# Performance work log

Hardware: AMD Instinct MI355X
Metric: run time of the kernel (lower is better)

The kernel has to match this reference:

```python
import jax, jax.numpy as jnp
import numpy as np

# Model constants (from source: model_dim=1024, head_dim=128, num_heads=8)
L = 8          # num layers (reduced from 16 for tractable reference memory)
T = 2048       # packed tokens, B == 1 (varlen)
DIM = 1024
NH = 8
NKV = 4        # GQA kv heads
HD = 128
KVD = NKV * HD
BLOCK = 128
WS = 3
WIN = WS * BLOCK           # sliding-window size for 'S' layers
ATTN_SCALE = 0.12
PATTERN = 'SSSL'
GATE_CH = 32
EPS = 1.1920929e-07        # torch F.rms_norm default eps = finfo(fp32).eps


def rms_norm(x):
    return x * jax.lax.rsqrt(jnp.mean(x * x, axis=-1, keepdims=True) + EPS)


def apply_rotary(x, cos, sin):
    # x: [T, H, HD]; cos/sin: [T, 1, HD//2]
    d = x.shape[-1] // 2
    x1, x2 = x[..., :d], x[..., d:]
    return jnp.concatenate([x1 * cos + x2 * sin, -x1 * sin + x2 * cos], axis=-1)


def has_ve(layer_idx, n_layer):
    return layer_idx % 2 == (n_layer - 1) % 2


def setup_inputs() -> dict:
    key = jax.random.key(0)
    ks = jax.random.split(key, 9)
    x = jax.random.normal(ks[0], (1, T, DIM), jnp.float32)
    ve = jax.random.normal(ks[1], (L, T, KVD), jnp.float32)
    s = DIM ** -0.5
    Wq = jax.random.normal(ks[2], (L, DIM, NH * HD), jnp.float32) * s
    Wk = jax.random.normal(ks[3], (L, DIM, KVD), jnp.float32) * s
    Wv = jax.random.normal(ks[4], (L, DIM, KVD), jnp.float32) * s
    Wo = jax.random.normal(ks[5], (L, NH * HD, DIM), jnp.float32) * (NH * HD) ** -0.5
    Wgate = jax.random.normal(ks[6], (L, GATE_CH, NKV), jnp.float32) * GATE_CH ** -0.5
    Wfc = jax.random.normal(ks[7], (L, DIM, 4 * DIM), jnp.float32) * s
    Wproj = jax.random.normal(ks[8], (L, 4 * DIM, DIM), jnp.float32) * (4 * DIM) ** -0.5
    # RoPE tables (absolute positions of the packed batch, as in the source)
    inv_freq = 1.0 / (10000.0 ** (jnp.arange(HD // 2, dtype=jnp.float32) / (HD // 2)))
    ang = jnp.arange(T, dtype=jnp.float32)[:, None] * inv_freq[None, :]
    cos = jnp.cos(ang)[:, None, :]
    sin = jnp.sin(ang)[:, None, :]
    # cu_seqlens: 4 packed documents of 512 tokens
    seqlens = jnp.array([0, 512, 1024, 1536, 2048], dtype=jnp.int32)
    return dict(x=x, ve=ve, Wq=Wq, Wk=Wk, Wv=Wv, Wo=Wo, Wgate=Wgate,
                Wfc=Wfc, Wproj=Wproj, cos=cos, sin=sin, seqlens=seqlens)


def reference(x, ve, Wq, Wk, Wv, Wo, Wgate, Wfc, Wproj, cos, sin, seqlens):
    h = x[0]  # [T, DIM], B == 1 (varlen packing)
    pos = jnp.arange(T)
    doc = jnp.searchsorted(seqlens, pos, side='right') - 1
    diff = pos[:, None] - pos[None, :]
    base = (diff >= 0) & (doc[:, None] == doc[None, :])   # causal within doc
    mask_S = base & (diff <= WIN)                         # sliding window
    neg = jnp.float32(-1e30)
    rep = NH // NKV
    for l in range(L):
        xn = rms_norm(h)
        q = (xn @ Wq[l]).reshape(T, NH, HD)
        k = (xn @ Wk[l]).reshape(T, NKV, HD)
        v = (xn @ Wv[l]).reshape(T, NKV, HD)
        if has_ve(l, L):
            gate = 2.0 * jax.nn.sigmoid(xn[:, :GATE_CH] @ Wgate[l])  # [T, NKV]
            v = v + gate[:, :, None] * ve[l].reshape(T, NKV, HD)
        q = rms_norm(apply_rotary(q, cos, sin))
        k = rms_norm(apply_rotary(k, cos, sin))
        k = jnp.repeat(k, rep, axis=1)   # GQA -> full heads
        v2 = jnp.repeat(v, rep, axis=1)
        scores = jnp.einsum('thd,shd->hts', q, k) * ATTN_SCALE  # [NH, T, T]
        mask = mask_S if PATTERN[l % len(PATTERN)] == 'S' else base
        scores = jnp.where(mask[None], scores, neg)
        p = jax.nn.softmax(scores, axis=-1)
        y = jnp.einsum('hts,shd->thd', p, v2).reshape(T, NH * HD)
        h = h + y @ Wo[l]
        m = jnp.square(jax.nn.relu(rms_norm(h) @ Wfc[l]))  # relu(x)^2 MLP
        h = h + m @ Wproj[l]
    return h[None]
```

## Files before the change

### kernel.cpp

```cpp
#include <hip/hip_runtime.h>
#include <hip/hip_bf16.h>
#include <cstdint>
#include <cstddef>

#define TT     2048
#define DMODEL 1024
#define NHQ    8
#define HD     128
#define KVD    512
#define WIN    384
#define EPSF   1.1920929e-07f
#define SCALE  0.12f

typedef __attribute__((ext_vector_type(8))) short bf16x8;
typedef __attribute__((ext_vector_type(4))) float f32x4;

#define WAITV(N)  asm volatile("s_waitcnt vmcnt(" #N ")" ::: "memory")

__device__ __forceinline__ float b2f(unsigned short u) {
    unsigned int i = ((unsigned int)u) << 16; float f; __builtin_memcpy(&f, &i, 4); return f;
}
__device__ __forceinline__ unsigned short f2b(float f) {
    unsigned int i; __builtin_memcpy(&i, &f, 4);
    unsigned int r = (i + 0x7fffu + ((i >> 16) & 1u)) >> 16;
    return (unsigned short)r;
}

__device__ __forceinline__ void gl_lds16(const unsigned short* g, unsigned short* l) {
    __builtin_amdgcn_global_load_lds(
        (const __attribute__((address_space(1))) unsigned int*)g,
        (__attribute__((address_space(3))) unsigned int*)l, 16, 0, 0);
}
__device__ __forceinline__ void gl_lds16f(const float* g, float* l) {
    __builtin_amdgcn_global_load_lds(
        (const __attribute__((address_space(1))) unsigned int*)g,
        (__attribute__((address_space(3))) unsigned int*)l, 16, 0, 0);
}

__global__ __launch_bounds__(512)
void convT_k(const float* __restrict__ Wq, const float* __restrict__ Wk,
             const float* __restrict__ Wv, const float* __restrict__ Wo,
             const float* __restrict__ Wfc, const float* __restrict__ Wproj,
             unsigned short* __restrict__ Bqkv, unsigned short* __restrict__ Bo,
             unsigned short* __restrict__ Bfc, unsigned short* __restrict__ Bproj)
{
    __shared__ float lt[128 * 128];
    const int bid = blockIdx.x, tid = threadIdx.x, l = blockIdx.y;

    const float* W; unsigned short* Wt; int K, N, t, nbase;
    if (bid < 64)         { W = Wq    + (size_t)l * 1024 * 1024; Wt = Bqkv  + (size_t)l * 2048 * 1024; K = 1024; N = 1024; t = bid;       nbase = 0;    }
    else if (bid < 96)    { W = Wk    + (size_t)l * 1024 * 512;  Wt = Bqkv  + (size_t)l * 2048 * 1024; K = 1024; N = 512;  t = bid - 64;  nbase = 1024; }
    else if (bid < 128)   { W = Wv    + (size_t)l * 1024 * 512;  Wt = Bqkv  + (size_t)l * 2048 * 1024; K = 1024; N = 512;  t = bid - 96;  nbase = 1536; }
    else if (bid < 192)   { W = Wo    + (size_t)l * 1024 * 1024; Wt = Bo    + (size_t)l * 1024 * 1024; K = 1024; N = 1024; t = bid - 128; nbase = 0;    }
    else if (bid < 448)   { W = Wfc   + (size_t)l * 1024 * 4096; Wt = Bfc   + (size_t)l * 4096 * 1024; K = 1024; N = 4096; t = bid - 192; nbase = 0;    }
    else                  { W = Wproj + (size_t)l * 4096 * 1024; Wt = Bproj + (size_t)l * 1024 * 4096; K = 4096; N = 1024; t = bid - 448; nbase = 0;    }

    const int ktiles = K >> 7;
    const int kt0 = (t % ktiles) * 128, nt0 = (t / ktiles) * 128;

    const int lane = tid & 63, w = tid >> 6;
    const int lhi = lane >> 5;
    const int lc  = lane & 31;

    #pragma unroll
    for (int rd = 0; rd < 8; ++rd) {
        const int k = rd * 16 + w * 2 + lhi;
        const int csrc = lc ^ ((k >> 3) & 31);
        const float* src = W + (size_t)(kt0 + k) * N + nt0 + csrc * 4;
        float* dst = lt + (size_t)(rd * 16 + w * 2) * 128;
        gl_lds16f(src, dst);
    }
    __syncthreads();

    #pragma unroll
    for (int i = 0; i < 4; ++i) {
        int flat = i * 512 + tid;
        int n = flat >> 4, kc = (flat & 15) * 8;
        const int c = ((n >> 2) ^ (kc >> 3)) & 31;
        const float* rp = lt + (size_t)kc * 128 + c * 4 + (n & 3);
        unsigned short o[8];
        #pragma unroll
        for (int j = 0; j < 8; ++j) o[j] = f2b(rp[j * 128]);
        *(uint4*)(Wt + (size_t)(nbase + nt0 + n) * K + kt0 + kc) = *(const uint4*)o;
    }
}

template<int EPI>
__global__ __launch_bounds__(256, 2)
void gemm4(const unsigned short* __restrict__ A, const unsigned short* __restrict__ Bt,
           unsigned short* __restrict__ Cp, int K, int ksplit, int Ntot)
{
    __shared__ unsigned short As[2 * 128 * 64];
    __shared__ unsigned short Bs[2 * 128 * 64];
    const int BUF = 128 * 64;
    const int tid = threadIdx.x, lane = tid & 63, wv = tid >> 6;

    const int gx = gridDim.x;
    const int nwg = gx * gridDim.y;
    const int ihw = blockIdx.y * gx + blockIdx.x;
    const int q = nwg >> 3, r = nwg & 7;
    const int xcd = ihw & 7, pos = ihw >> 3;
    const int lg = (xcd < r) ? xcd * (q + 1) + pos
                             : r * (q + 1) + (xcd - r) * q + pos;
    const int m0 = (lg % gx) * 128, n0 = (lg / gx) * 128;

    const int kbeg = blockIdx.z * ksplit;
    const int NT = ksplit >> 6;

    const int wr = (wv >> 1) * 64, wc = (wv & 1) * 64;
    const int l15 = lane & 15, g = lane >> 4;
    const int srow = lane >> 3;
    const int sxor = (((lane & 7) ^ srow) << 3);

    const unsigned short* gA0 = A  + (size_t)(m0 + wv * 32 + srow) * K + sxor;
    const unsigned short* gB0 = Bt + (size_t)(n0 + wv * 32 + srow) * K + sxor;

    auto stage = [&](int t) {
        const int b = t & 1;
        const size_t k = (size_t)kbeg + ((size_t)t << 6);
        unsigned short* la = As + b * BUF + (wv * 32) * 64;
        unsigned short* lb = Bs + b * BUF + (wv * 32) * 64;
        #pragma unroll
        for (int c = 0; c < 4; ++c) {
            gl_lds16(gA0 + (size_t)(c * 8) * K + k, la + c * 8 * 64);
            gl_lds16(gB0 + (size_t)(c * 8) * K + k, lb + c * 8 * 64);
        }
    };

    f32x4 acc[4][4] = {};

    stage(0);
    for (int t = 0; t < NT; ++t) {
        if (t + 1 < NT) { stage(t + 1); WAITV(8); }
        else            { WAITV(0); }
        __builtin_amdgcn_s_barrier();

        const unsigned short* Ac = As + (t & 1) * BUF;
        const unsigned short* Bc = Bs + (t & 1) * BUF;
        bf16x8 af[4][2], bfv[4][2];
        #pragma unroll
        for (int mi = 0; mi < 4; ++mi) {
            const int row = wr + mi * 16 + l15, x = row & 7;
            #pragma unroll
            for (int kk = 0; kk < 2; ++kk)
                af[mi][kk] = *(const bf16x8*)(Ac + row * 64 + (((kk * 4 + g) ^ x) << 3));
        }
        #pragma unroll
        for (int ni = 0; ni < 4; ++ni) {
            const int row = wc + ni * 16 + l15, x = row & 7;
            #pragma unroll
            for (int kk = 0; kk < 2; ++kk)
                bfv[ni][kk] = *(const bf16x8*)(Bc + row * 64 + (((kk * 4 + g) ^ x) << 3));
        }
        __builtin_amdgcn_s_setprio(1);
        #pragma unroll
        for (int kk = 0; kk < 2; ++kk)
            #pragma unroll
            for (int mi = 0; mi < 4; ++mi)
                #pragma unroll
                for (int ni = 0; ni < 4; ++ni)
                    acc[mi][ni] = __builtin_amdgcn_mfma_f32_16x16x32_bf16(af[mi][kk], bfv[ni][kk], acc[mi][ni], 0, 0, 0);
        __builtin_amdgcn_s_setprio(0);
        __builtin_amdgcn_s_barrier();
    }

    unsigned short* Cz = Cp + (size_t)blockIdx.z * TT * Ntot;
    #pragma unroll
    for (int mi = 0; mi < 4; ++mi)
        #pragma unroll
        for (int ni = 0; ni < 4; ++ni)
            #pragma unroll
            for (int r2 = 0; r2 < 4; ++r2) {
                int row = m0 + wr + mi * 16 + g * 4 + r2;
                int col = n0 + wc + ni * 16 + l15;
                size_t idx = (size_t)row * Ntot + col;
                float v = acc[mi][ni][r2];
                if (EPI == 0) Cz[idx] = f2b(v);
                else {
                    float z = v > 0.f ? v * v : 0.f;
                    Cz[idx] = f2b(z);
                }
            }
}

__global__ __launch_bounds__(256)
void rmsnormF_k(float* __restrict__ h, const unsigned short* __restrict__ part, int nz,
                unsigned short* __restrict__ xn)
{
    const int t = blockIdx.x, tid = threadIdx.x;
    const size_t idx = (size_t)t * (DMODEL / 4) + tid;
    float4 v = ((const float4*)h)[idx];
    for (int z = 0; z < nz; ++z) {
        ushort4 p = ((const ushort4*)part)[idx + (size_t)z * (TT * DMODEL / 4)];
        v.x += b2f(p.x); v.y += b2f(p.y); v.z += b2f(p.z); v.w += b2f(p.w);
    }
    if (nz > 0) ((float4*)h)[idx] = v;

    float ss = v.x*v.x + v.y*v.y + v.z*v.z + v.w*v.w;
    #pragma unroll
    for (int m = 1; m < 64; m <<= 1) ss += __shfl_xor(ss, m);
    __shared__ float red[4];
    if ((tid & 63) == 0) red[tid >> 6] = ss;
    __syncthreads();
    float tot = red[0] + red[1] + red[2] + red[3];
    float rs = rsqrtf(tot * (1.f / DMODEL) + EPSF);
    unsigned short o[4] = { f2b(v.x*rs), f2b(v.y*rs), f2b(v.z*rs), f2b(v.w*rs) };
    *(ushort4*)(xn + (size_t)t * DMODEL + tid * 4) = *(const ushort4*)o;
}

__global__ __launch_bounds__(256)
void reduce_add_k(float* __restrict__ h, const unsigned short* __restrict__ part, int nz)
{
    const int i = blockIdx.x * 256 + threadIdx.x;
    float4 hv = ((float4*)h)[i];
    for (int z = 0; z < nz; ++z) {
        ushort4 p = ((const ushort4*)part)[i + (size_t)z * (TT * DMODEL / 4)];
        hv.x += b2f(p.x); hv.y += b2f(p.y); hv.z += b2f(p.z); hv.w += b2f(p.w);
    }
    ((float4*)h)[i] = hv;
}

__global__ __launch_bounds__(128)
void post_qkv_k(const unsigned short* __restrict__ qkv,
                const float* __restrict__ cosb, const float* __restrict__ sinb,
                unsigned short* __restrict__ qn, unsigned short* __restrict__ kn)
{
    const size_t S2 = (size_t)TT * 2048;
    const int t = blockIdx.x, tid = threadIdx.x;
    __shared__ float cs[64], sn[64];
    if (tid < 64) { cs[tid] = cosb[t * 64 + tid]; sn[tid] = sinb[t * 64 + tid]; }
    __syncthreads();
    if (tid < 96) {
        const int hid = tid >> 3, sub = tid & 7;
        const unsigned short* src; unsigned short* dst;
        if (hid < 8) { src = qkv + (size_t)t * 2048 + hid * 128;              dst = qn + (size_t)t * 1024 + hid * 128; }
        else         { src = qkv + (size_t)t * 2048 + 1024 + (hid - 8) * 128; dst = kn + (size_t)t * 512 + (hid - 8) * 128; }
        float o1[8], o2[8], ssum = 0.f;
        #pragma unroll
        for (int j = 0; j < 8; ++j) {
            int jj = sub * 8 + j;
            float x1 = b2f(src[jj])      + b2f(src[jj + S2]);
            float x2 = b2f(src[jj + 64]) + b2f(src[jj + 64 + S2]);
            float c = cs[jj], s = sn[jj];
            o1[j] = x1 * c + x2 * s;
            o2[j] = -x1 * s + x2 * c;
            ssum += o1[j]*o1[j] + o2[j]*o2[j];
        }
        ssum += __shfl_xor(ssum, 1); ssum += __shfl_xor(ssum, 2); ssum += __shfl_xor(ssum, 4);
        float rs = rsqrtf(ssum * (1.f / HD) + EPSF);
        #pragma unroll
        for (int j = 0; j < 8; ++j) {
            int jj = sub * 8 + j;
            dst[jj]      = f2b(o1[j] * rs);
            dst[jj + 64] = f2b(o2[j] * rs);
        }
    }
}

__global__ __launch_bounds__(256)
void vtrans2_k(const unsigned short* __restrict__ qkv, const unsigned short* __restrict__ xn,
               const float* __restrict__ Wgate, const float* __restrict__ vel, int hasve,
               unsigned short* __restrict__ vt)
{
    const size_t S2 = (size_t)TT * 2048;
    __shared__ unsigned short lt[64][72];
    __shared__ float gate_s[64];
    const int t0 = blockIdx.x * 64, c0 = blockIdx.y * 64, tid = threadIdx.x;
    const int gi = c0 >> 7;

    if (hasve && tid < 64) {
        const int t = t0 + tid;
        float a = 0.f;
        #pragma unroll
        for (int c = 0; c < 32; ++c) a += b2f(xn[(size_t)t * DMODEL + c]) * Wgate[c * 4 + gi];
        gate_s[tid] = 2.f / (1.f + __expf(-a));
    }
    __syncthreads();

    #pragma unroll
    for (int i = 0; i < 2; ++i) {
        int r = (tid >> 3) + i * 32;
        int c = (tid & 7) * 8;
        const int t = t0 + r, ch = c0 + c;
        size_t off = (size_t)t * 2048 + 1536 + ch;
        bf16x8 pa = *(const bf16x8*)(qkv + off);
        bf16x8 pb = *(const bf16x8*)(qkv + off + S2);
        float g = hasve ? gate_s[r] : 0.f;
        #pragma unroll
        for (int j = 0; j < 8; ++j) {
            float vv = b2f(((unsigned short*)&pa)[j]) + b2f(((unsigned short*)&pb)[j]);
            if (hasve) vv += g * vel[(size_t)t * KVD + ch + j];
            lt[c + j][r] = f2b(vv);
        }
    }
    __syncthreads();
    #pragma unroll
    for (int i = 0; i < 2; ++i) {
        int r = (tid >> 3) + i * 32;
        int c = (tid & 7) * 8;
        *(bf16x8*)(vt + (size_t)(c0 + r) * TT + t0 + c) = *(const bf16x8*)(&lt[r][c]);
    }
}

__global__ __launch_bounds__(256)
void attn_k(const unsigned short* __restrict__ qn, const unsigned short* __restrict__ kn,
            const unsigned short* __restrict__ vt,
            float* __restrict__ pacc, float* __restrict__ pml,
            const int* __restrict__ seqlens, int isS)
{
    const int tid = threadIdx.x, w = tid >> 6, lane = tid & 63;
    const int h = blockIdx.y, hkv = h >> 1, z = blockIdx.z;
    const int qr = (blockIdx.x * 4 + w) * 16;
    const int s1 = seqlens[1], s2 = seqlens[2], s3 = seqlens[3];
    const int l15 = lane & 15, g = lane >> 4;

    const int row = qr + l15;
    const int drow = (row >= s1) + (row >= s2) + (row >= s3);

    int dq = (qr >= s1) + (qr >= s2) + (qr >= s3);
    int dstart = dq == 0 ? 0 : (dq == 1 ? s1 : (dq == 2 ? s2 : s3));
    int smin = dstart;
    if (isS) { int wlo = qr - WIN; if (wlo > smin) smin = wlo; }
    if (smin < 0) smin = 0;
    const int smax = qr + 16;

    const int base0 = smin & ~31;
    const int ntiles = (smax - base0 + 31) >> 5;
    const int tp = (ntiles + 1) >> 1;
    const int tbeg = z ? tp : 0, tend = z ? ntiles : tp;

    const size_t rowi = ((size_t)z * NHQ + h) * TT + row;

    if (tbeg >= tend) {
        if (lane < 16) { pml[rowi * 2] = -1e30f; pml[rowi * 2 + 1] = 0.f; }
        return;
    }

    bf16x8 qf[4];
    #pragma unroll
    for (int kk = 0; kk < 4; ++kk)
        qf[kk] = *(const bf16x8*)(qn + (size_t)(qr + l15) * 1024 + h * HD + kk * 32 + g * 8);

    f32x4 acc[8] = {};
    float mrow = -1e30f, lrow = 0.f;

    for (int tt = tbeg; tt < tend; ++tt) {
        const int s0 = base0 + tt * 32;
        f32x4 S[2] = {};
        __builtin_amdgcn_s_setprio(1);
        #pragma unroll
        for (int nb = 0; nb < 2; ++nb) {
            int srow = s0 + nb * 16 + l15;
            #pragma unroll
            for (int kk = 0; kk < 4; ++kk) {
                bf16x8 kf = *(const bf16x8*)(kn + (size_t)srow * KVD + hkv * HD + kk * 32 + g * 8);
                S[nb] = __builtin_amdgcn_mfma_f32_16x16x32_bf16(kf, qf[kk], S[nb], 0, 0, 0);
            }
        }
        __builtin_amdgcn_s_setprio(0);

        float sv[2][4];
        #pragma unroll
        for (int nb = 0; nb < 2; ++nb)
            #pragma unroll
            for (int r = 0; r < 4; ++r) {
                int s = s0 + nb * 16 + 4 * g + r;
                int dcol = (s >= s1) + (s >= s2) + (s >= s3);
                bool valid = (s <= row) && (dcol == drow) && (!isS || (row - s) <= WIN);
                sv[nb][r] = valid ? S[nb][r] * SCALE : -1e30f;
            }

        float pm = sv[0][0];
        #pragma unroll
        for (int r = 1; r < 4; ++r) pm = fmaxf(pm, sv[0][r]);
        #pragma unroll
        for (int r = 0; r < 4; ++r) pm = fmaxf(pm, sv[1][r]);
        pm = fmaxf(pm, __shfl_xor(pm, 16));
        pm = fmaxf(pm, __shfl_xor(pm, 32));
        float mnew = fmaxf(mrow, pm);
        const float vany = (mnew > -1e29f) ? 1.f : 0.f;
        float scl2 = __expf(mrow - mnew);
        float p0[4], p1[4], ps = 0.f;
        #pragma unroll
        for (int r = 0; r < 4; ++r) {
            p0[r] = vany * __expf(sv[0][r] - mnew);
            p1[r] = vany * __expf(sv[1][r] - mnew);
            ps += p0[r] + p1[r];
        }
        ps += __shfl_xor(ps, 16);
        ps += __shfl_xor(ps, 32);
        lrow = lrow * scl2 + ps;
        mrow = mnew;
        #pragma unroll
        for (int nb2 = 0; nb2 < 8; ++nb2) acc[nb2] *= scl2;

        unsigned short pt[8];
        const int base = l15 + ((g & 1) << 5);
        #pragma unroll
        for (int jh = 0; jh < 2; ++jh)
            #pragma unroll
            for (int r = 0; r < 4; ++r) {
                float ta = __shfl(p0[r], base + 16 * jh);
                float tb = __shfl(p1[r], base + 16 * jh);
                pt[jh * 4 + r] = f2b(g >= 2 ? tb : ta);
            }
        bf16x8 pf;
        #pragma unroll
        for (int j = 0; j < 8; ++j) ((unsigned short*)&pf)[j] = pt[j];

        __builtin_amdgcn_s_setprio(1);
        #pragma unroll
        for (int nb2 = 0; nb2 < 8; ++nb2) {
            bf16x8 vf = *(const bf16x8*)(vt + (size_t)(hkv * HD + nb2 * 16 + l15) * TT + s0 + g * 8);
            acc[nb2] = __builtin_amdgcn_mfma_f32_16x16x32_bf16(vf, pf, acc[nb2], 0, 0, 0);
        }
        __builtin_amdgcn_s_setprio(0);
    }

    float* pa = pacc + rowi * HD;
    #pragma unroll
    for (int nb2 = 0; nb2 < 8; ++nb2)
        *(float4*)(pa + nb2 * 16 + 4 * g) = *(float4*)&acc[nb2];
    if (lane < 16) { pml[rowi * 2] = mrow; pml[rowi * 2 + 1] = lrow; }
}

__global__ __launch_bounds__(256)
void attn_merge_k(const float* __restrict__ pacc, const float* __restrict__ pml,
                  unsigned short* __restrict__ y)
{
    const int r = blockIdx.x, tid = threadIdx.x;
    const int h = tid >> 5, dg = (tid & 31) * 4;
    const size_t i1 = ((size_t)0 * NHQ + h) * TT + r;
    const size_t i2 = ((size_t)1 * NHQ + h) * TT + r;
    const float m1 = pml[i1 * 2], l1 = pml[i1 * 2 + 1];
    const float m2 = pml[i2 * 2], l2 = pml[i2 * 2 + 1];
    const float M = fmaxf(m1, m2);
    const float w1 = (l1 > 0.f) ? __expf(m1 - M) : 0.f;
    const float w2 = (l2 > 0.f) ? __expf(m2 - M) : 0.f;
    const float inv = 1.f / (w1 * l1 + w2 * l2);

    float4 a1 = {0.f, 0.f, 0.f, 0.f}, a2 = {0.f, 0.f, 0.f, 0.f};
    if (l1 > 0.f) a1 = *(const float4*)(pacc + i1 * HD + dg);
    if (l2 > 0.f) a2 = *(const float4*)(pacc + i2 * HD + dg);

    unsigned short o[4];
    o[0] = f2b((w1 * a1.x + w2 * a2.x) * inv);
    o[1] = f2b((w1 * a1.y + w2 * a2.y) * inv);
    o[2] = f2b((w1 * a1.z + w2 * a2.z) * inv);
    o[3] = f2b((w1 * a1.w + w2 * a2.w) * inv);
    *(ushort4*)(y + (size_t)r * 1024 + h * HD + dg) = *(const ushort4*)o;
}

extern "C" void kernel_launch(void* const* d_in, const int* in_sizes, int n_in,
                              void* d_out, int out_size, void* d_ws, size_t ws_size,
                              hipStream_t stream)
{
    const float* x       = (const float*)d_in[0];
    const float* ve      = (const float*)d_in[1];
    const float* Wq      = (const float*)d_in[2];
    const float* Wk      = (const float*)d_in[3];
    const float* Wv      = (const float*)d_in[4];
    const float* Wo      = (const float*)d_in[5];
    const float* Wgate   = (const float*)d_in[6];
    const float* Wfc     = (const float*)d_in[7];
    const float* Wproj   = (const float*)d_in[8];
    const float* cosb    = (const float*)d_in[9];
    const float* sinb    = (const float*)d_in[10];
    const int*   seqlens = (const int*)d_in[11];

    float* h = (float*)d_out;
    char* ws = (char*)d_ws;
    unsigned short* xn    = (unsigned short*)(ws);
    unsigned short* qn    = (unsigned short*)(ws + (4ull  << 20));
    unsigned short* kn    = (unsigned short*)(ws + (8ull  << 20));
    unsigned short* vt    = (unsigned short*)(ws + (12ull << 20));
    unsigned short* yb    = (unsigned short*)(ws + (14ull << 20));
    unsigned short* mb    = (unsigned short*)(ws + (18ull << 20));
    unsigned short* part  = (unsigned short*)(ws + (34ull << 20));
    float*          pacc  = (float*)(ws + (50ull << 20));
    float*          pml   = (float*)(ws + (66ull << 20));
    unsigned short* Bqkv  = (unsigned short*)(ws + (68ull  << 20));
    unsigned short* Bo    = (unsigned short*)(ws + (100ull << 20));
    unsigned short* Bfc   = (unsigned short*)(ws + (116ull << 20));
    unsigned short* Bproj = (unsigned short*)(ws + (180ull << 20));

    hipMemcpyAsync(h, x, (size_t)TT * DMODEL * sizeof(float), hipMemcpyDeviceToDevice, stream);

    convT_k<<<dim3(704, 8), 512, 0, stream>>>(Wq, Wk, Wv, Wo, Wfc, Wproj,
                                              Bqkv, Bo, Bfc, Bproj);

    for (int l = 0; l < 8; ++l) {
        int hasve = (l % 2) == 1;
        int isS   = (l % 4) != 3;

        rmsnormF_k<<<TT, 256, 0, stream>>>(h, part, l == 0 ? 0 : 4, xn);

        gemm4<0><<<dim3(16, 16, 2), 256, 0, stream>>>(xn, Bqkv + (size_t)l * 2048 * 1024,
                                                      part, 1024, 512, 2048);

        post_qkv_k<<<TT, 128, 0, stream>>>(part, cosb, sinb, qn, kn);

        vtrans2_k<<<dim3(32, 8), 256, 0, stream>>>(part, xn,
            Wgate + (size_t)l * 128, ve + (size_t)l * TT * KVD, hasve, vt);

        attn_k<<<dim3(32, 8, 2), 256, 0, stream>>>(qn, kn, vt, pacc, pml, seqlens, isS);
        attn_merge_k<<<TT, 256, 0, stream>>>(pacc, pml, yb);

        gemm4<0><<<dim3(16, 8, 4), 256, 0, stream>>>(yb, Bo + (size_t)l * 1024 * 1024,
                                                     part, 1024, 256, 1024);

        rmsnormF_k<<<TT, 256, 0, stream>>>(h, part, 4, xn);

        gemm4<2><<<dim3(16, 32, 1), 256, 0, stream>>>(xn, Bfc + (size_t)l * 4096 * 1024,
                                                      mb, 1024, 1024, 4096);

        gemm4<0><<<dim3(16, 8, 4), 256, 0, stream>>>(mb, Bproj + (size_t)l * 1024 * 4096,
                                                     part, 4096, 1024, 1024);
    }

    reduce_add_k<<<2048, 256, 0, stream>>>(h, part, 4);
}
```

Before: 1.269 ms.

## Add gemm10 with XCD-aware tile remap and double split-K for small GEMMs

Adds a new GEMM kernel, gemm10, with double-buffered direct global-to-LDS staging, an XCD-aware remapping of workgroup indices to tiles, and MFMA priority raising. It also doubles the split-K factor for the QKV, O and proj GEMMs so more workgroups fill the GPU. Every consumer of the partial buffers now sums 4 or 8 bf16 partials instead of 2 or 4, and the workspace layout is shifted to fit the larger partial buffer. The trade-off is more partial-sum traffic and more bf16 rounding steps in exchange for better occupancy on the small-N GEMMs.

Result: slower. 1.424 ms (+12.2%).

```diff
diff --git a/kernel.cpp b/kernel.cpp
--- a/kernel.cpp
+++ b/kernel.cpp
@@ -183,6 +183,98 @@
             }
 }
 
+template<int EPI>
+__global__ __launch_bounds__(256, 4)
+void gemm10(const unsigned short* __restrict__ A, const unsigned short* __restrict__ Bt,
+            unsigned short* __restrict__ Cp, int K, int ksplit, int Ntot)
+{
+    __shared__ unsigned short As[2 * 128 * 32];
+    __shared__ unsigned short Bs[2 * 128 * 32];
+    const int BUF = 128 * 32;
+    const int tid = threadIdx.x, lane = tid & 63, wv = tid >> 6;
+
+    const int gx = gridDim.x;
+    const int nwg = gx * gridDim.y;
+    const int ihw = blockIdx.y * gx + blockIdx.x;
+    const int q = nwg >> 3, r = nwg & 7;
+    const int xcd = ihw & 7, pos = ihw >> 3;
+    const int lg = (xcd < r) ? xcd * (q + 1) + pos
+                             : r * (q + 1) + (xcd - r) * q + pos;
+    const int m0 = (lg % gx) * 128, n0 = (lg / gx) * 128;
+
+    const int kbeg = blockIdx.z * ksplit;
+    const int NT = ksplit >> 5;
+
+    const int wr = (wv >> 1) * 64, wc = (wv & 1) * 64;
+    const int l15 = lane & 15, g = lane >> 4;
+    const int srow = lane >> 2;
+    const int schunk = (((lane & 3) ^ ((lane >> 3) & 3)) << 3);
+
+    const unsigned short* gA0 = A  + (size_t)(m0 + wv * 32 + srow) * K + schunk;
+    const unsigned short* gB0 = Bt + (size_t)(n0 + wv * 32 + srow) * K + schunk;
+
+    auto stage = [&](int t) {
+        const int b = t & 1;
+        const size_t k = (size_t)kbeg + ((size_t)t << 5);
+        unsigned short* la = As + b * BUF + (wv * 32) * 32;
+        unsigned short* lb = Bs + b * BUF + (wv * 32) * 32;
+        #pragma unroll
+        for (int c = 0; c < 2; ++c) {
+            gl_lds16(gA0 + (size_t)(c * 16) * K + k, la + c * 16 * 32);
+            gl_lds16(gB0 + (size_t)(c * 16) * K + k, lb + c * 16 * 32);
+        }
+    };
+
+    f32x4 acc[4][4] = {};
+
+    stage(0);
+    for (int t = 0; t < NT; ++t) {
+        if (t + 1 < NT) { stage(t + 1); WAITV(4); }
+        else            { WAITV(0); }
+        __builtin_amdgcn_s_barrier();
+
+        const unsigned short* Ac = As + (t & 1) * BUF;
+        const unsigned short* Bc = Bs + (t & 1) * BUF;
+        bf16x8 af[4], bfv[4];
+        #pragma unroll
+        for (int mi = 0; mi < 4; ++mi) {
+            const int row = wr + mi * 16 + l15, x = (row >> 1) & 3;
+            af[mi] = *(const bf16x8*)(Ac + row * 32 + ((g ^ x) << 3));
+        }
+        #pragma unroll
+        for (int ni = 0; ni < 4; ++ni) {
+            const int row = wc + ni * 16 + l15, x = (row >> 1) & 3;
+            bfv[ni] = *(const bf16x8*)(Bc + row * 32 + ((g ^ x) << 3));
+        }
+        __builtin_amdgcn_s_setprio(1);
+        #pragma unroll
+        for (int mi = 0; mi < 4; ++mi)
+            #pragma unroll
+            for (int ni = 0; ni < 4; ++ni)
+                acc[mi][ni] = __builtin_amdgcn_mfma_f32_16x16x32_bf16(af[mi], bfv[ni], acc[mi][ni], 0, 0, 0);
+        __builtin_amdgcn_s_setprio(0);
+        __builtin_amdgcn_s_barrier();
+    }
+
+    unsigned short* Cz = Cp + (size_t)blockIdx.z * TT * Ntot;
+    #pragma unroll
+    for (int mi = 0; mi < 4; ++mi)
+        #pragma unroll
+        for (int ni = 0; ni < 4; ++ni)
+            #pragma unroll
+            for (int r2 = 0; r2 < 4; ++r2) {
+                int row = m0 + wr + mi * 16 + g * 4 + r2;
+                int col = n0 + wc + ni * 16 + l15;
+                size_t idx = (size_t)row * Ntot + col;
+                float v = acc[mi][ni][r2];
+                if (EPI == 0) Cz[idx] = f2b(v);
+                else {
+                    float z = v > 0.f ? v * v : 0.f;
+                    Cz[idx] = f2b(z);
+                }
+            }
+}
+
 __global__ __launch_bounds__(256)
 void rmsnormF_k(float* __restrict__ h, const unsigned short* __restrict__ part, int nz,
                 unsigned short* __restrict__ xn)
@@ -239,8 +331,10 @@
         #pragma unroll
         for (int j = 0; j < 8; ++j) {
             int jj = sub * 8 + j;
-            float x1 = b2f(src[jj])      + b2f(src[jj + S2]);
-            float x2 = b2f(src[jj + 64]) + b2f(src[jj + 64 + S2]);
+            float x1 = b2f(src[jj])      + b2f(src[jj + S2])
+                     + b2f(src[jj + 2*S2]) + b2f(src[jj + 3*S2]);
+            float x2 = b2f(src[jj + 64]) + b2f(src[jj + 64 + S2])
+                     + b2f(src[jj + 64 + 2*S2]) + b2f(src[jj + 64 + 3*S2]);
             float c = cs[jj], s = sn[jj];
             o1[j] = x1 * c + x2 * s;
             o2[j] = -x1 * s + x2 * c;
@@ -283,12 +377,15 @@
         int c = (tid & 7) * 8;
         const int t = t0 + r, ch = c0 + c;
         size_t off = (size_t)t * 2048 + 1536 + ch;
-        bf16x8 pa = *(const bf16x8*)(qkv + off);
-        bf16x8 pb = *(const bf16x8*)(qkv + off + S2);
+        bf16x8 p0 = *(const bf16x8*)(qkv + off);
+        bf16x8 p1 = *(const bf16x8*)(qkv + off + S2);
+        bf16x8 p2 = *(const bf16x8*)(qkv + off + 2*S2);
+        bf16x8 p3 = *(const bf16x8*)(qkv + off + 3*S2);
         float g = hasve ? gate_s[r] : 0.f;
         #pragma unroll
         for (int j = 0; j < 8; ++j) {
-            float vv = b2f(((unsigned short*)&pa)[j]) + b2f(((unsigned short*)&pb)[j]);
+            float vv = b2f(((unsigned short*)&p0)[j]) + b2f(((unsigned short*)&p1)[j])
+                     + b2f(((unsigned short*)&p2)[j]) + b2f(((unsigned short*)&p3)[j]);
             if (hasve) vv += g * vel[(size_t)t * KVD + ch + j];
             lt[c + j][r] = f2b(vv);
         }
@@ -471,18 +568,18 @@
     float* h = (float*)d_out;
     char* ws = (char*)d_ws;
     unsigned short* xn    = (unsigned short*)(ws);
-    unsigned short* qn    = (unsigned short*)(ws + (4ull  << 20));
-    unsigned short* kn    = (unsigned short*)(ws + (8ull  << 20));
-    unsigned short* vt    = (unsigned short*)(ws + (12ull << 20));
-    unsigned short* yb    = (unsigned short*)(ws + (14ull << 20));
-    unsigned short* mb    = (unsigned short*)(ws + (18ull << 20));
-    unsigned short* part  = (unsigned short*)(ws + (34ull << 20));
-    float*          pacc  = (float*)(ws + (50ull << 20));
-    float*          pml   = (float*)(ws + (66ull << 20));
-    unsigned short* Bqkv  = (unsigned short*)(ws + (68ull  << 20));
-    unsigned short* Bo    = (unsigned short*)(ws + (100ull << 20));
-    unsigned short* Bfc   = (unsigned short*)(ws + (116ull << 20));
-    unsigned short* Bproj = (unsigned short*)(ws + (180ull << 20));
+    unsigned short* qn    = (unsigned short*)(ws + (4ull   << 20));
+    unsigned short* kn    = (unsigned short*)(ws + (8ull   << 20));
+    unsigned short* vt    = (unsigned short*)(ws + (10ull  << 20));
+    float*          pml   = (float*)(ws + (12ull  << 20));
+    unsigned short* yb    = (unsigned short*)(ws + (13ull  << 20));
+    unsigned short* mb    = (unsigned short*)(ws + (17ull  << 20));
+    unsigned short* part  = (unsigned short*)(ws + (33ull  << 20));
+    float*          pacc  = (float*)(ws + (65ull  << 20));
+    unsigned short* Bqkv  = (unsigned short*)(ws + (81ull  << 20));
+    unsigned short* Bo    = (unsigned short*)(ws + (113ull << 20));
+    unsigned short* Bfc   = (unsigned short*)(ws + (129ull << 20));
+    unsigned short* Bproj = (unsigned short*)(ws + (193ull << 20));
 
     hipMemcpyAsync(h, x, (size_t)TT * DMODEL * sizeof(float), hipMemcpyDeviceToDevice, stream);
 
@@ -493,10 +590,10 @@
         int hasve = (l % 2) == 1;
         int isS   = (l % 4) != 3;
 
-        rmsnormF_k<<<TT, 256, 0, stream>>>(h, part, l == 0 ? 0 : 4, xn);
-
-        gemm4<0><<<dim3(16, 16, 2), 256, 0, stream>>>(xn, Bqkv + (size_t)l * 2048 * 1024,
-                                                      part, 1024, 512, 2048);
+        rmsnormF_k<<<TT, 256, 0, stream>>>(h, part, l == 0 ? 0 : 8, xn);
+
+        gemm10<0><<<dim3(16, 16, 4), 256, 0, stream>>>(xn, Bqkv + (size_t)l * 2048 * 1024,
+                                                       part, 1024, 256, 2048);
 
         post_qkv_k<<<TT, 128, 0, stream>>>(part, cosb, sinb, qn, kn);
 
@@ -506,17 +603,17 @@
         attn_k<<<dim3(32, 8, 2), 256, 0, stream>>>(qn, kn, vt, pacc, pml, seqlens, isS);
         attn_merge_k<<<TT, 256, 0, stream>>>(pacc, pml, yb);
 
-        gemm4<0><<<dim3(16, 8, 4), 256, 0, stream>>>(yb, Bo + (size_t)l * 1024 * 1024,
-                                                     part, 1024, 256, 1024);
-
-        rmsnormF_k<<<TT, 256, 0, stream>>>(h, part, 4, xn);
+        gemm10<0><<<dim3(16, 8, 8), 256, 0, stream>>>(yb, Bo + (size_t)l * 1024 * 1024,
+                                                      part, 1024, 128, 1024);
+
+        rmsnormF_k<<<TT, 256, 0, stream>>>(h, part, 8, xn);
 
         gemm4<2><<<dim3(16, 32, 1), 256, 0, stream>>>(xn, Bfc + (size_t)l * 4096 * 1024,
                                                       mb, 1024, 1024, 4096);
 
-        gemm4<0><<<dim3(16, 8, 4), 256, 0, stream>>>(mb, Bproj + (size_t)l * 1024 * 4096,
-                                                     part, 4096, 1024, 1024);
-    }
-
-    reduce_add_k<<<2048, 256, 0, stream>>>(h, part, 4);
-}
+        gemm10<0><<<dim3(16, 8, 8), 256, 0, stream>>>(mb, Bproj + (size_t)l * 1024 * 4096,
+                                                      part, 4096, 512, 1024);
+    }
+
+    reduce_add_k<<<2048, 256, 0, stream>>>(h, part, 8);
+}
```
